# Optimization experiments

Measured on AMD Instinct MI355X. Metric: run time of the kernel, lower is better.

## Reference

```python
import jax, jax.numpy as jnp
import numpy as np

D_MODEL, H, DK = 768, 12, 64
RQ, RK, RV = 6, 2, 2
B, S = 8, 4096


def setup_inputs() -> dict:
    key = jax.random.key(0)
    ks = jax.random.split(key, 16)
    def lin(k, din, dout):
        k1, k2 = jax.random.split(k)
        s = 1.0 / np.sqrt(din)
        W = jax.random.uniform(k1, (din, dout), jnp.float32, -s, s)
        b = jax.random.uniform(k2, (dout,), jnp.float32, -s, s)
        return W, b
    W_a_q, b_a_q = lin(ks[0], D_MODEL, H * RQ)
    W_b_q, b_b_q = lin(ks[1], D_MODEL, DK * RQ)
    W_a_k, b_a_k = lin(ks[2], D_MODEL, H * RK)
    W_b_k, b_b_k = lin(ks[3], D_MODEL, DK * RK)
    W_a_v, b_a_v = lin(ks[4], D_MODEL, H * RV)
    W_b_v, b_b_v = lin(ks[5], D_MODEL, DK * RV)
    W_out, b_out = lin(ks[6], H * DK, D_MODEL)
    x = jax.random.normal(ks[7], (B, S, D_MODEL), jnp.float32)
    rope_pos = jax.random.normal(ks[8], (S, DK), jnp.float32)
    return {
        "x": x, "rope_pos": rope_pos,
        "W_a_q": W_a_q, "b_a_q": b_a_q, "W_b_q": W_b_q, "b_b_q": b_b_q,
        "W_a_k": W_a_k, "b_a_k": b_a_k, "W_b_k": W_b_k, "b_b_k": b_b_k,
        "W_a_v": W_a_v, "b_a_v": b_a_v, "W_b_v": W_b_v, "b_b_v": b_b_v,
        "W_out": W_out, "b_out": b_out,
    }


def reference(x, rope_pos, W_a_q, b_a_q, W_b_q, b_b_q, W_a_k, b_a_k,
              W_b_k, b_b_k, W_a_v, b_a_v, W_b_v, b_b_v, W_out, b_out):
    b, s, _ = x.shape
    # factor projections; layout (B, S, rank, feature)
    A_Q = (x @ W_a_q + b_a_q).reshape(b, s, RQ, H)
    B_Q = (x @ W_b_q + b_b_q).reshape(b, s, RQ, DK)
    A_K = (x @ W_a_k + b_a_k).reshape(b, s, RK, H)
    B_K = (x @ W_b_k + b_b_k).reshape(b, s, RK, DK)
    A_V = (x @ W_a_v + b_a_v).reshape(b, s, RV, H)
    B_V = (x @ W_b_v + b_b_v).reshape(b, s, RV, DK)
    rope = rope_pos[None, :, None, :]  # (1,S,1,DK)
    B_Q = B_Q * rope
    B_K = B_K * rope
    # rank-sum outer products -> (B,S,H,DK)
    Q = jnp.einsum('bsrh,bsrd->bshd', A_Q, B_Q)
    K = jnp.einsum('bsrh,bsrd->bshd', A_K, B_K)
    V = jnp.einsum('bsrh,bsrd->bshd', A_V, B_V)
    # faithful to original: scores over head dim, shape (B,S,H,H)
    scores = jnp.einsum('bshd,bsgd->bshg', Q, K) / jnp.sqrt(jnp.float32(DK))
    attn = jax.nn.softmax(scores, axis=-1)
    out = jnp.einsum('bshg,bsgd->bshd', attn, V)  # (B,S,H,DK)
    # faithful reshape: (B,S,H,DK) -> transpose(1,2) -> (B,H,S,DK) -> view (B,S,H*DK)
    out = jnp.transpose(out, (0, 2, 1, 3)).reshape(b, s, H * DK)
    return out @ W_out + b_out
```

## Files before the change

kernel.cpp:

```cpp
#include <hip/hip_runtime.h>
#include <hip/hip_bf16.h>

#define D_MODEL 768
#define NH 12
#define DK 64
#define RQ 6
#define RK 2
#define RV 2
#define BATCH 8
#define SEQ 4096
#define NPOS (BATCH*SEQ)

typedef _Float16 v8h __attribute__((ext_vector_type(8)));
typedef float v4f __attribute__((ext_vector_type(4)));

__global__ __launch_bounds__(256) void repack(
    const float* __restrict__ Waq, const float* __restrict__ baq,
    const float* __restrict__ Wbq, const float* __restrict__ bbq,
    const float* __restrict__ Wak, const float* __restrict__ bak,
    const float* __restrict__ Wbk, const float* __restrict__ bbk,
    const float* __restrict__ Wav, const float* __restrict__ bav,
    const float* __restrict__ Wbv, const float* __restrict__ bbv,
    const float* __restrict__ Wo,
    _Float16* __restrict__ WcatT, _Float16* __restrict__ WoT,
    float* __restrict__ bcat)
{
    const int n = blockIdx.x;
    const int t = threadIdx.x;
    const float* W = nullptr; const float* bsrc = nullptr;
    int cols = 0, col = 0;
    if      (n <  72) { W=Waq; bsrc=baq; cols=72;  col=n;     }
    else if (n < 456) { W=Wbq; bsrc=bbq; cols=384; col=n-72;  }
    else if (n < 480) { W=Wak; bsrc=bak; cols=24;  col=n-456; }
    else if (n < 608) { W=Wbk; bsrc=bbk; cols=128; col=n-480; }
    else if (n < 632) { W=Wav; bsrc=bav; cols=24;  col=n-608; }
    else if (n < 760) { W=Wbv; bsrc=bbv; cols=128; col=n-632; }
    for (int k = t; k < 768; k += 256) {
        WcatT[(size_t)n*768 + k] = W ? (_Float16)W[(size_t)k*cols + col] : (_Float16)0.f;
        WoT[(size_t)n*768 + k]   = (_Float16)Wo[(size_t)k*768 + n];
    }
    if (t == 0) bcat[n] = W ? bsrc[col] : 0.f;
}

#define LSTR 129
template<int MODE>
__global__ __launch_bounds__(256) void mfma_gemm(
    const void* __restrict__ Aptr,
    const _Float16* __restrict__ BT,
    const float* __restrict__ bias,
    const float* __restrict__ rope,
    float* __restrict__ C)
{
    const int t = threadIdx.x;
    const int lane = t & 63;
    const int wave = t >> 6;

    const int flat = blockIdx.y * 6 + blockIdx.x;
    const int xcd = flat & 7;
    const int sub = flat >> 3;
    const int ct  = sub % 6;
    const int rt  = xcd * 32 + sub / 6;
    const int row0 = rt * 128;
    const int col0 = ct * 128;

    const int wrow = (wave >> 1) * 64;
    const int wcol = (wave & 1) * 64;

    __shared__ v8h As[4*LSTR];
    __shared__ v8h Bs[4*LSTR];

    v4f acc[4][4];
    #pragma unroll
    for (int i = 0; i < 4; ++i)
        #pragma unroll
        for (int j = 0; j < 4; ++j)
            acc[i][j] = (v4f){0.f, 0.f, 0.f, 0.f};

    const v8h* gB = (const v8h*)BT;
    const float4* gA32 = (const float4*)Aptr;
    const v8h* gA16 = (const v8h*)Aptr;

    const int arow = t >> 2;
    const int akc  = t & 3;

    const int q = lane >> 4;
    const int m = lane & 15;

    for (int k0 = 0; k0 < 768; k0 += 32) {
        __syncthreads();
        #pragma unroll
        for (int rh = 0; rh < 2; ++rh) {
            const int row = arow + rh*64;
            if (MODE == 0) {
                float4 f0 = gA32[(size_t)(row0 + row)*192 + (k0>>2) + akc*2];
                float4 f1 = gA32[(size_t)(row0 + row)*192 + (k0>>2) + akc*2 + 1];
                v8h h;
                h[0]=(_Float16)f0.x; h[1]=(_Float16)f0.y; h[2]=(_Float16)f0.z; h[3]=(_Float16)f0.w;
                h[4]=(_Float16)f1.x; h[5]=(_Float16)f1.y; h[6]=(_Float16)f1.z; h[7]=(_Float16)f1.w;
                As[akc*LSTR + row] = h;
            } else {
                As[akc*LSTR + row] = gA16[(size_t)(row0 + row)*96 + (k0>>3) + akc];
            }
            Bs[akc*LSTR + row] = gB[(size_t)(col0 + row)*96 + (k0>>3) + akc];
        }
        __syncthreads();

        v8h af[4], bf[4];
        #pragma unroll
        for (int mi = 0; mi < 4; ++mi)
            af[mi] = As[q*LSTR + wrow + mi*16 + m];
        #pragma unroll
        for (int ni = 0; ni < 4; ++ni)
            bf[ni] = Bs[q*LSTR + wcol + ni*16 + m];
        #pragma unroll
        for (int mi = 0; mi < 4; ++mi)
            #pragma unroll
            for (int ni = 0; ni < 4; ++ni)
                acc[mi][ni] = __builtin_amdgcn_mfma_f32_16x16x32_f16(
                    af[mi], bf[ni], acc[mi][ni], 0, 0, 0);
    }

    #pragma unroll
    for (int mi = 0; mi < 4; ++mi) {
        #pragma unroll
        for (int i = 0; i < 4; ++i) {
            const int grow = row0 + wrow + mi*16 + q*4 + i;
            #pragma unroll
            for (int ni = 0; ni < 4; ++ni) {
                const int gcol = col0 + wcol + ni*16 + m;
                float v = acc[mi][ni][i] + bias[gcol];
                if (MODE == 0) {
                    const int s = grow & 4095;
                    if (gcol >= 72 && gcol < 456)
                        v *= rope[s*64 + ((gcol - 72) & 63)];
                    else if (gcol >= 480 && gcol < 608)
                        v *= rope[s*64 + ((gcol - 480) & 63)];
                }
                C[(size_t)grow*768 + gcol] = v;
            }
        }
    }
}

__global__ __launch_bounds__(256) void tpa_attn_f(
    const float* __restrict__ P,
    _Float16* __restrict__ O)
{
    const int t = threadIdx.x;
    const int pos0 = blockIdx.x * 8;

    __shared__ float proj[8][772];
    __shared__ float Gs[8][12];
    __shared__ float sc[8][160];
    __shared__ float cs[8][24];

    const float4* gp = (const float4*)P;
    for (int i = t; i < 8*192; i += 256) {
        int p = i / 192, c = i - p*192;
        float4 u = gp[(size_t)(pos0 + p)*192 + c];
        proj[p][c*4+0] = u.x; proj[p][c*4+1] = u.y;
        proj[p][c*4+2] = u.z; proj[p][c*4+3] = u.w;
    }
    __syncthreads();

    if (t < 96) {
        int p = t / 12, u = t - (t/12)*12, r = u >> 1, r2 = u & 1;
        const float* bq = &proj[p][72  + r*64];
        const float* bk = &proj[p][480 + r2*64];
        const int ph = (r*8 + r2*16) & 63;
        float acc = 0.f;
        for (int i = 0; i < 64; ++i) {
            int d = (i + ph) & 63;
            acc = fmaf(bq[d], bk[d], acc);
        }
        Gs[p][u] = acc * 0.125f;
    }
    __syncthreads();

    for (int i = t; i < 8*144; i += 256) {
        int p = i / 144, v = i - p*144, h = v / 12, g = v - (v/12)*12;
        float s = 0.f;
        #pragma unroll
        for (int r = 0; r < RQ; ++r) {
            float mg = fmaf(Gs[p][r*2+1], proj[p][468 + g],
                            Gs[p][r*2+0] * proj[p][456 + g]);
            s = fmaf(proj[p][r*12 + h], mg, s);
        }
        sc[p][h*13 + g] = s;
    }
    __syncthreads();

    if (t < 96) {
        int p = t / 12, h = t - (t/12)*12;
        float* row = &sc[p][h*13];
        float mx = -1e30f;
        #pragma unroll
        for (int g = 0; g < NH; ++g) mx = fmaxf(mx, row[g]);
        float sum = 0.f;
        #pragma unroll
        for (int g = 0; g < NH; ++g) { float e = __expf(row[g]-mx); row[g] = e; sum += e; }
        float inv = 1.0f / sum;
        #pragma unroll
        for (int g = 0; g < NH; ++g) row[g] *= inv;
    }
    __syncthreads();

    if (t < 192) {
        int p = t / 24, u = t - (t/24)*24, h = u >> 1, r2 = u & 1;
        float acc = 0.f;
        #pragma unroll
        for (int g = 0; g < NH; ++g)
            acc = fmaf(sc[p][h*13+g], proj[p][608 + r2*12 + g], acc);
        cs[p][h*2 + r2] = acc;
    }
    __syncthreads();

    for (int i = t; i < 8*768; i += 256) {
        int p = i / 768, j = i - p*768, h = j >> 6, d = j & 63;
        int pos = pos0 + p, b = pos >> 12, s = pos & 4095;
        float val = fmaf(cs[p][h*2+1], proj[p][632 + 64 + d],
                         cs[p][h*2+0] * proj[p][632 + d]);
        O[(((size_t)b*NH + h)*SEQ + s)*DK + d] = (_Float16)val;
    }
}

extern "C" void kernel_launch(void* const* d_in, const int* in_sizes, int n_in,
                              void* d_out, int out_size, void* d_ws, size_t ws_size,
                              hipStream_t stream) {
    const float* x    = (const float*)d_in[0];
    const float* rope = (const float*)d_in[1];
    const float* Waq  = (const float*)d_in[2];
    const float* baq  = (const float*)d_in[3];
    const float* Wbq  = (const float*)d_in[4];
    const float* bbq  = (const float*)d_in[5];
    const float* Wak  = (const float*)d_in[6];
    const float* bak  = (const float*)d_in[7];
    const float* Wbk  = (const float*)d_in[8];
    const float* bbk  = (const float*)d_in[9];
    const float* Wav  = (const float*)d_in[10];
    const float* bav  = (const float*)d_in[11];
    const float* Wbv  = (const float*)d_in[12];
    const float* bbv  = (const float*)d_in[13];
    const float* Wo   = (const float*)d_in[14];
    const float* bo   = (const float*)d_in[15];

    char* ws = (char*)d_ws;
    _Float16* WcatT = (_Float16*)(ws);
    _Float16* WoT   = (_Float16*)(ws + 1179648);
    float*    bcat  = (float*)(ws + 2359296);
    _Float16* O     = (_Float16*)(ws + 2363392);

    float* P = (float*)d_out;

    repack<<<768, 256, 0, stream>>>(Waq, baq, Wbq, bbq, Wak, bak, Wbk, bbk,
                                    Wav, bav, Wbv, bbv, Wo, WcatT, WoT, bcat);

    dim3 gg(6, 256);
    mfma_gemm<0><<<gg, 256, 0, stream>>>(x, WcatT, bcat, rope, P);

    tpa_attn_f<<<NPOS/8, 256, 0, stream>>>(P, O);

    mfma_gemm<1><<<gg, 256, 0, stream>>>(O, WoT, bo, nullptr, (float*)d_out);
}
```

Baseline: 398.9 us.

## Pre-convert x to fp16, use async global-to-LDS loads, store projections in fp16

Adds a separate kernel that converts x to fp16 once, so the projection GEMM can load fp16 tiles directly into LDS with global_load_lds and a K-step of 64 instead of converting per tile. The projection output is written in fp16 instead of fp32, which halves the intermediate traffic read by the attention kernel. Both fp16 buffers are placed in the output buffer as scratch. This costs an extra pass over x and lowers the precision of the intermediate projections, and the new LDS layout has no padding, so bank conflicts are possible.

```diff
diff --git a/kernel.cpp b/kernel.cpp
--- a/kernel.cpp
+++ b/kernel.cpp
@@ -13,6 +13,26 @@
 
 typedef _Float16 v8h __attribute__((ext_vector_type(8)));
 typedef float v4f __attribute__((ext_vector_type(4)));
+
+__device__ __forceinline__ void async16(const _Float16* g, _Float16* l) {
+    __builtin_amdgcn_global_load_lds(
+        (const __attribute__((address_space(1))) _Float16*)g,
+        (__attribute__((address_space(3))) _Float16*)l, 16, 0, 0);
+}
+
+__global__ __launch_bounds__(256) void cvt_fp16(
+    const float4* __restrict__ x, v8h* __restrict__ xh, int nchunks)
+{
+    int i = blockIdx.x * 256 + threadIdx.x;
+    const int stride = gridDim.x * 256;
+    for (; i < nchunks; i += stride) {
+        float4 a = x[(size_t)i*2], b = x[(size_t)i*2 + 1];
+        v8h h;
+        h[0]=(_Float16)a.x; h[1]=(_Float16)a.y; h[2]=(_Float16)a.z; h[3]=(_Float16)a.w;
+        h[4]=(_Float16)b.x; h[5]=(_Float16)b.y; h[6]=(_Float16)b.z; h[7]=(_Float16)b.w;
+        xh[i] = h;
+    }
+}
 
 __global__ __launch_bounds__(256) void repack(
     const float* __restrict__ Waq, const float* __restrict__ baq,
@@ -42,14 +62,13 @@
     if (t == 0) bcat[n] = W ? bsrc[col] : 0.f;
 }
 
-#define LSTR 129
 template<int MODE>
 __global__ __launch_bounds__(256) void mfma_gemm(
-    const void* __restrict__ Aptr,
+    const _Float16* __restrict__ A,
     const _Float16* __restrict__ BT,
     const float* __restrict__ bias,
     const float* __restrict__ rope,
-    float* __restrict__ C)
+    void* __restrict__ Cout)
 {
     const int t = threadIdx.x;
     const int lane = t & 63;
@@ -65,9 +84,11 @@
 
     const int wrow = (wave >> 1) * 64;
     const int wcol = (wave & 1) * 64;
-
-    __shared__ v8h As[4*LSTR];
-    __shared__ v8h Bs[4*LSTR];
+    const int q = lane >> 4;
+    const int m = lane & 15;
+
+    __shared__ _Float16 As[8*128*8];
+    __shared__ _Float16 Bs[8*128*8];
 
     v4f acc[4][4];
     #pragma unroll
@@ -76,48 +97,40 @@
         for (int j = 0; j < 4; ++j)
             acc[i][j] = (v4f){0.f, 0.f, 0.f, 0.f};
 
+    const v8h* gA = (const v8h*)A;
     const v8h* gB = (const v8h*)BT;
-    const float4* gA32 = (const float4*)Aptr;
-    const v8h* gA16 = (const v8h*)Aptr;
-
-    const int arow = t >> 2;
-    const int akc  = t & 3;
-
-    const int q = lane >> 4;
-    const int m = lane & 15;
-
-    for (int k0 = 0; k0 < 768; k0 += 32) {
+
+    for (int k0 = 0; k0 < 768; k0 += 64) {
+        const int kb = k0 >> 3;
         __syncthreads();
         #pragma unroll
-        for (int rh = 0; rh < 2; ++rh) {
-            const int row = arow + rh*64;
-            if (MODE == 0) {
-                float4 f0 = gA32[(size_t)(row0 + row)*192 + (k0>>2) + akc*2];
-                float4 f1 = gA32[(size_t)(row0 + row)*192 + (k0>>2) + akc*2 + 1];
-                v8h h;
-                h[0]=(_Float16)f0.x; h[1]=(_Float16)f0.y; h[2]=(_Float16)f0.z; h[3]=(_Float16)f0.w;
-                h[4]=(_Float16)f1.x; h[5]=(_Float16)f1.y; h[6]=(_Float16)f1.z; h[7]=(_Float16)f1.w;
-                As[akc*LSTR + row] = h;
-            } else {
-                As[akc*LSTR + row] = gA16[(size_t)(row0 + row)*96 + (k0>>3) + akc];
-            }
-            Bs[akc*LSTR + row] = gB[(size_t)(col0 + row)*96 + (k0>>3) + akc];
+        for (int j = 0; j < 4; ++j) {
+            const int id = wave*4 + j;
+            const int kc = id & 7;
+            const int hf = id >> 3;
+            async16((const _Float16*)(gA + (size_t)(row0 + hf*64 + lane)*96 + kb + kc),
+                    &As[(kc*128 + hf*64)*8]);
+            async16((const _Float16*)(gB + (size_t)(col0 + hf*64 + lane)*96 + kb + kc),
+                    &Bs[(kc*128 + hf*64)*8]);
         }
         __syncthreads();
 
-        v8h af[4], bf[4];
-        #pragma unroll
-        for (int mi = 0; mi < 4; ++mi)
-            af[mi] = As[q*LSTR + wrow + mi*16 + m];
-        #pragma unroll
-        for (int ni = 0; ni < 4; ++ni)
-            bf[ni] = Bs[q*LSTR + wcol + ni*16 + m];
-        #pragma unroll
-        for (int mi = 0; mi < 4; ++mi)
+        #pragma unroll
+        for (int ss = 0; ss < 2; ++ss) {
+            v8h af[4], bf[4];
+            #pragma unroll
+            for (int mi = 0; mi < 4; ++mi)
+                af[mi] = *(const v8h*)&As[((ss*4 + q)*128 + wrow + mi*16 + m)*8];
             #pragma unroll
             for (int ni = 0; ni < 4; ++ni)
-                acc[mi][ni] = __builtin_amdgcn_mfma_f32_16x16x32_f16(
-                    af[mi], bf[ni], acc[mi][ni], 0, 0, 0);
+                bf[ni] = *(const v8h*)&Bs[((ss*4 + q)*128 + wcol + ni*16 + m)*8];
+            #pragma unroll
+            for (int mi = 0; mi < 4; ++mi)
+                #pragma unroll
+                for (int ni = 0; ni < 4; ++ni)
+                    acc[mi][ni] = __builtin_amdgcn_mfma_f32_16x16x32_f16(
+                        af[mi], bf[ni], acc[mi][ni], 0, 0, 0);
+        }
     }
 
     #pragma unroll
@@ -135,15 +148,17 @@
                         v *= rope[s*64 + ((gcol - 72) & 63)];
                     else if (gcol >= 480 && gcol < 608)
                         v *= rope[s*64 + ((gcol - 480) & 63)];
+                    ((_Float16*)Cout)[(size_t)grow*768 + gcol] = (_Float16)v;
+                } else {
+                    ((float*)Cout)[(size_t)grow*768 + gcol] = v;
                 }
-                C[(size_t)grow*768 + gcol] = v;
             }
         }
     }
 }
 
 __global__ __launch_bounds__(256) void tpa_attn_f(
-    const float* __restrict__ P,
+    const _Float16* __restrict__ P,
     _Float16* __restrict__ O)
 {
     const int t = threadIdx.x;
@@ -154,12 +169,12 @@
     __shared__ float sc[8][160];
     __shared__ float cs[8][24];
 
-    const float4* gp = (const float4*)P;
-    for (int i = t; i < 8*192; i += 256) {
-        int p = i / 192, c = i - p*192;
-        float4 u = gp[(size_t)(pos0 + p)*192 + c];
-        proj[p][c*4+0] = u.x; proj[p][c*4+1] = u.y;
-        proj[p][c*4+2] = u.z; proj[p][c*4+3] = u.w;
+    const v8h* gp = (const v8h*)P;
+    for (int i = t; i < 8*96; i += 256) {
+        int p = i / 96, c = i - p*96;
+        v8h u = gp[(size_t)(pos0 + p)*96 + c];
+        #pragma unroll
+        for (int j = 0; j < 8; ++j) proj[p][c*8+j] = (float)u[j];
     }
     __syncthreads();
 
@@ -250,15 +265,18 @@
     float*    bcat  = (float*)(ws + 2359296);
     _Float16* O     = (_Float16*)(ws + 2363392);
 
-    float* P = (float*)d_out;
+    _Float16* xh = (_Float16*)d_out;
+    _Float16* P  = (_Float16*)((char*)d_out + 50331648);
+
+    cvt_fp16<<<3072, 256, 0, stream>>>((const float4*)x, (v8h*)xh, NPOS*96);
 
     repack<<<768, 256, 0, stream>>>(Waq, baq, Wbq, bbq, Wak, bak, Wbk, bbk,
                                     Wav, bav, Wbv, bbv, Wo, WcatT, WoT, bcat);
 
     dim3 gg(6, 256);
-    mfma_gemm<0><<<gg, 256, 0, stream>>>(x, WcatT, bcat, rope, P);
+    mfma_gemm<0><<<gg, 256, 0, stream>>>(xh, WcatT, bcat, rope, P);
 
     tpa_attn_f<<<NPOS/8, 256, 0, stream>>>(P, O);
 
-    mfma_gemm<1><<<gg, 256, 0, stream>>>(O, WoT, bo, nullptr, (float*)d_out);
-}
+    mfma_gemm<1><<<gg, 256, 0, stream>>>(O, WoT, bo, nullptr, d_out);
+}
```

New measurement: 444.0 us. +11.3%, slower.
